# Kernel tuning notes

Hardware: AMD Instinct MI355X
Metric: run time of the kernel (lower is better)

Reference implementation:

```python
import jax, jax.numpy as jnp
import numpy as np

T = 2048        # flattened tokens (one prefill sequence)
HID = 2048      # hidden_size
NH = 32         # query heads
NKV = 4         # kv heads
HD = 128        # head_dim
THETA = 1000000.0
EPS = 1e-6


def setup_inputs() -> dict:
    key = jax.random.key(0)
    k0, k1, k2 = jax.random.split(key, 3)
    return {
        "positions": jnp.arange(T, dtype=jnp.int32),
        "hidden_states": jax.random.normal(k0, (T, HID), dtype=jnp.float32),
        "w_qkv": jax.random.normal(k1, ((NH + 2 * NKV) * HD, HID), dtype=jnp.float32) * 0.02,
        "w_o": jax.random.normal(k2, (HID, NH * HD), dtype=jnp.float32) * 0.02,
        "q_norm_w": jnp.ones((HD,), dtype=jnp.float32),
        "k_norm_w": jnp.ones((HD,), dtype=jnp.float32),
    }


def _rmsnorm(x, w):
    # per-head RMSNorm over last dim (head_dim), fp32 math
    var = jnp.mean(x * x, axis=-1, keepdims=True)
    return x * jax.lax.rsqrt(var + EPS) * w


def _rope(x, positions):
    # NeoX-style rotary embedding over full head_dim
    d = x.shape[-1]
    inv_freq = 1.0 / (THETA ** (jnp.arange(0, d, 2, dtype=jnp.float32) / d))  # [d/2]
    ang = positions.astype(jnp.float32)[:, None] * inv_freq                   # [T, d/2]
    cos = jnp.cos(ang)[:, None, :]  # [T,1,d/2]
    sin = jnp.sin(ang)[:, None, :]
    x1, x2 = jnp.split(x, 2, axis=-1)
    return jnp.concatenate([x1 * cos - x2 * sin, x2 * cos + x1 * sin], axis=-1)


def reference(positions, hidden_states, w_qkv, w_o, q_norm_w, k_norm_w):
    # fused QKV projection (no bias)
    qkv = hidden_states @ w_qkv.T                       # [T, (NH+2*NKV)*HD]
    q, k, v = jnp.split(qkv, [NH * HD, (NH + NKV) * HD], axis=-1)
    q = _rmsnorm(q.reshape(T, NH, HD), q_norm_w)        # [T,NH,HD]
    k = _rmsnorm(k.reshape(T, NKV, HD), k_norm_w)       # [T,NKV,HD]
    v = v.reshape(T, NKV, HD)
    q = _rope(q, positions)
    k = _rope(k, positions)
    # GQA: expand kv heads to query heads
    g = NH // NKV
    k = jnp.repeat(k, g, axis=1)                        # [T,NH,HD]
    v = jnp.repeat(v, g, axis=1)
    scale = HD ** -0.5
    scores = jnp.einsum('qhd,khd->hqk', q, k) * scale   # [NH,T,T]
    causal = jnp.tril(jnp.ones((T, T), dtype=bool))
    scores = jnp.where(causal[None, :, :], scores, jnp.finfo(scores.dtype).min)
    attn = jax.nn.softmax(scores, axis=-1)
    o = jnp.einsum('hqk,khd->qhd', attn, v).reshape(T, NH * HD)
    return o @ w_o.T                                    # [T,HID]
```

## Files before the change

kernel.cpp:

```cpp
#include <hip/hip_runtime.h>
#include <math.h>

#define T 2048
#define HID 2048
#define NH 32
#define NKV 4
#define HD 128
#define QKV_DIM 5120
#define OD 4096
#define C2LOG 0.12751743f
#define MFIX 6.0f

typedef _Float16 half8 __attribute__((ext_vector_type(8)));
typedef _Float16 half4v __attribute__((ext_vector_type(4)));
typedef float floatx4 __attribute__((ext_vector_type(4)));

#define GLD16(gp, lp) __builtin_amdgcn_global_load_lds( \
    (const __attribute__((address_space(1))) void*)(gp), \
    (__attribute__((address_space(3))) void*)(lp), 16, 0, 0)

__global__ __launch_bounds__(256)
void cvt_all(const float* __restrict__ h, const float* __restrict__ wq,
             const float* __restrict__ wo, _Float16* __restrict__ out) {
    size_t i = ((size_t)blockIdx.x * 256 + threadIdx.x) * 4;
    const float* src;
    size_t off;
    if (i < (size_t)T * HID)                        { src = h;  off = i; }
    else if (i < (size_t)T * HID + (size_t)QKV_DIM * HID)
                                                    { src = wq; off = i - (size_t)T * HID; }
    else                                            { src = wo; off = i - (size_t)T * HID - (size_t)QKV_DIM * HID; }
    float4 v = *(const float4*)(src + off);
    half4v o = { (_Float16)v.x, (_Float16)v.y, (_Float16)v.z, (_Float16)v.w };
    *(half4v*)(out + i) = o;
}

__global__ __launch_bounds__(256)
void gemm_sk_h(const _Float16* __restrict__ A, const _Float16* __restrict__ B,
               _Float16* __restrict__ p0, _Float16* __restrict__ p1,
               int M, int N, int K, int KS) {
    __shared__ __align__(16) _Float16 Asm[8192];
    __shared__ __align__(16) _Float16 Bsm[8192];
    int tid = threadIdx.x;
    int wave = tid >> 6, lane = tid & 63;
    int quad = lane >> 4, l16 = lane & 15;
    int m0 = blockIdx.y * 128, n0 = blockIdx.x * 128;
    int koff = blockIdx.z * KS;
    _Float16* C = blockIdx.z ? p1 : p0;
    int wm = (wave >> 1) * 64, wn = (wave & 1) * 64;
    const _Float16* Ag = A + (size_t)(m0 + (tid >> 2)) * K + koff + (tid & 3) * 8;
    const _Float16* Bg = B + (size_t)(n0 + (tid >> 2)) * K + koff + (tid & 3) * 8;
    size_t row64 = (size_t)64 * K;
    int wofs = wave * 512;
    floatx4 acc[4][4] = {};
    int nt = KS >> 5;
    GLD16(Ag, Asm + wofs);
    GLD16(Ag + row64, Asm + 2048 + wofs);
    GLD16(Bg, Bsm + wofs);
    GLD16(Bg + row64, Bsm + 2048 + wofs);
    for (int t = 0; t < nt; t++) {
        int cur = t & 1;
        if (t + 1 < nt) {
            const _Float16* Agp = Ag + (size_t)(t + 1) * 32;
            const _Float16* Bgp = Bg + (size_t)(t + 1) * 32;
            int nb = (cur ^ 1) * 4096 + wofs;
            GLD16(Agp, Asm + nb);
            GLD16(Agp + row64, Asm + nb + 2048);
            GLD16(Bgp, Bsm + nb);
            GLD16(Bgp + row64, Bsm + nb + 2048);
            asm volatile("s_waitcnt vmcnt(4)" ::: "memory");
        } else {
            asm volatile("s_waitcnt vmcnt(0)" ::: "memory");
        }
        __builtin_amdgcn_s_barrier();
        __builtin_amdgcn_sched_barrier(0);
        int pb = cur * 4096;
        half8 af[4], bf[4];
        #pragma unroll
        for (int i = 0; i < 4; i++)
            af[i] = *(const half8*)&Asm[pb + (wm + i * 16 + l16) * 32 + quad * 8];
        #pragma unroll
        for (int j = 0; j < 4; j++)
            bf[j] = *(const half8*)&Bsm[pb + (wn + j * 16 + l16) * 32 + quad * 8];
        #pragma unroll
        for (int i = 0; i < 4; i++)
            #pragma unroll
            for (int j = 0; j < 4; j++)
                acc[i][j] = __builtin_amdgcn_mfma_f32_16x16x32_f16(af[i], bf[j], acc[i][j], 0, 0, 0);
        __builtin_amdgcn_s_barrier();
    }
    #pragma unroll
    for (int i = 0; i < 4; i++) {
        int row = m0 + wm + i * 16 + quad * 4;
        #pragma unroll
        for (int j = 0; j < 4; j++) {
            int col = n0 + wn + j * 16 + l16;
            #pragma unroll
            for (int r = 0; r < 4; r++)
                C[(size_t)(row + r) * N + col] = (_Float16)acc[i][j][r];
        }
    }
}

__global__ __launch_bounds__(256)
void gemm_sk_f(const _Float16* __restrict__ A, const _Float16* __restrict__ B,
               _Float16* __restrict__ p0, _Float16* __restrict__ p1,
               _Float16* __restrict__ p2, _Float16* __restrict__ p3,
               int M, int N, int K, int KS) {
    __shared__ __align__(16) _Float16 Asm[8192];
    __shared__ __align__(16) _Float16 Bsm[8192];
    int tid = threadIdx.x;
    int wave = tid >> 6, lane = tid & 63;
    int quad = lane >> 4, l16 = lane & 15;
    int m0 = blockIdx.y * 128, n0 = blockIdx.x * 128;
    int bz = blockIdx.z;
    int koff = bz * KS;
    _Float16* C = (bz == 0) ? p0 : (bz == 1) ? p1 : (bz == 2) ? p2 : p3;
    int wm = (wave >> 1) * 64, wn = (wave & 1) * 64;
    const _Float16* Ag = A + (size_t)(m0 + (tid >> 2)) * K + koff + (tid & 3) * 8;
    const _Float16* Bg = B + (size_t)(n0 + (tid >> 2)) * K + koff + (tid & 3) * 8;
    size_t row64 = (size_t)64 * K;
    int wofs = wave * 512;
    floatx4 acc[4][4] = {};
    int nt = KS >> 5;
    GLD16(Ag, Asm + wofs);
    GLD16(Ag + row64, Asm + 2048 + wofs);
    GLD16(Bg, Bsm + wofs);
    GLD16(Bg + row64, Bsm + 2048 + wofs);
    for (int t = 0; t < nt; t++) {
        int cur = t & 1;
        if (t + 1 < nt) {
            const _Float16* Agp = Ag + (size_t)(t + 1) * 32;
            const _Float16* Bgp = Bg + (size_t)(t + 1) * 32;
            int nb = (cur ^ 1) * 4096 + wofs;
            GLD16(Agp, Asm + nb);
            GLD16(Agp + row64, Asm + nb + 2048);
            GLD16(Bgp, Bsm + nb);
            GLD16(Bgp + row64, Bsm + nb + 2048);
            asm volatile("s_waitcnt vmcnt(4)" ::: "memory");
        } else {
            asm volatile("s_waitcnt vmcnt(0)" ::: "memory");
        }
        __builtin_amdgcn_s_barrier();
        __builtin_amdgcn_sched_barrier(0);
        int pb = cur * 4096;
        half8 af[4], bf[4];
        #pragma unroll
        for (int i = 0; i < 4; i++)
            af[i] = *(const half8*)&Asm[pb + (wm + i * 16 + l16) * 32 + quad * 8];
        #pragma unroll
        for (int j = 0; j < 4; j++)
            bf[j] = *(const half8*)&Bsm[pb + (wn + j * 16 + l16) * 32 + quad * 8];
        #pragma unroll
        for (int i = 0; i < 4; i++)
            #pragma unroll
            for (int j = 0; j < 4; j++)
                acc[i][j] = __builtin_amdgcn_mfma_f32_16x16x32_f16(af[i], bf[j], acc[i][j], 0, 0, 0);
        __builtin_amdgcn_s_barrier();
    }
    #pragma unroll
    for (int i = 0; i < 4; i++) {
        int row = m0 + wm + i * 16 + quad * 4;
        #pragma unroll
        for (int j = 0; j < 4; j++) {
            int col = n0 + wn + j * 16 + l16;
            #pragma unroll
            for (int r = 0; r < 4; r++)
                C[(size_t)(row + r) * N + col] = (_Float16)acc[i][j][r];
        }
    }
}

__global__ __launch_bounds__(256)
void reduce4(const _Float16* __restrict__ p0, const _Float16* __restrict__ p1,
             const _Float16* __restrict__ p2, const _Float16* __restrict__ p3,
             float* __restrict__ out) {
    size_t i = ((size_t)blockIdx.x * 256 + threadIdx.x) * 4;
    half4v a = *(const half4v*)(p0 + i);
    half4v b = *(const half4v*)(p1 + i);
    half4v c = *(const half4v*)(p2 + i);
    half4v d = *(const half4v*)(p3 + i);
    float4 o = { (float)a.x + (float)b.x + (float)c.x + (float)d.x,
                 (float)a.y + (float)b.y + (float)c.y + (float)d.y,
                 (float)a.z + (float)b.z + (float)c.z + (float)d.z,
                 (float)a.w + (float)b.w + (float)c.w + (float)d.w };
    *(float4*)(out + i) = o;
}

__global__ __launch_bounds__(256)
void qkv_post(const _Float16* __restrict__ qp0, const _Float16* __restrict__ qp1,
              const int* __restrict__ positions,
              const float* __restrict__ qw, const float* __restrict__ kw,
              _Float16* __restrict__ Qb, _Float16* __restrict__ Kb,
              _Float16* __restrict__ Vt) {
    int t = blockIdx.x;
    int wave = threadIdx.x >> 6, lane = threadIdx.x & 63;
    float pos = (float)positions[t];
    float f = exp2f(-(float)lane * (19.9315685693241741f / 64.0f));
    float ang = pos * f;
    float s = sinf(ang), c = cosf(ang);
    const _Float16* r0 = qp0 + (size_t)t * QKV_DIM;
    const _Float16* r1 = qp1 + (size_t)t * QKV_DIM;
    for (int hh = wave; hh < NH + 2 * NKV; hh += 4) {
        float x1 = (float)r0[hh * HD + lane] + (float)r1[hh * HD + lane];
        float x2 = (float)r0[hh * HD + lane + 64] + (float)r1[hh * HD + lane + 64];
        if (hh < NH + NKV) {
            float ss = x1 * x1 + x2 * x2;
            for (int o = 1; o < 64; o <<= 1) ss += __shfl_xor(ss, o);
            float inv = rsqrtf(ss * (1.0f / HD) + 1e-6f);
            const float* w = (hh < NH) ? qw : kw;
            x1 = x1 * inv * w[lane];
            x2 = x2 * inv * w[lane + 64];
            float y1 = x1 * c - x2 * s;
            float y2 = x2 * c + x1 * s;
            _Float16* dst;
            if (hh < NH) dst = Qb + ((size_t)hh * T + t) * HD;
            else         dst = Kb + ((size_t)(hh - NH) * T + t) * HD;
            dst[lane]      = (_Float16)y1;
            dst[lane + 64] = (_Float16)y2;
        } else {
            int hk = hh - NH - NKV;
            Vt[((size_t)hk * HD + lane) * T + t]      = (_Float16)x1;
            Vt[((size_t)hk * HD + lane + 64) * T + t] = (_Float16)x2;
        }
    }
}

__global__ __launch_bounds__(256, 4)
void attn(const _Float16* __restrict__ Qb, const _Float16* __restrict__ Kb,
          const _Float16* __restrict__ Vt, _Float16* __restrict__ Ob) {
    __shared__ __align__(16) _Float16 Ksm[8192];
    __shared__ __align__(16) _Float16 Vsm[8192];
    __shared__ __align__(16) _Float16 Psm[4][1024];
    int b = blockIdx.x;
    int h = b & 31;
    int quarter = b >> 8;
    int i = (b & 255) >> 5;
    int qt = (quarter == 0) ? 31 - i : (quarter == 1) ? i
           : (quarter == 2) ? 23 - i : 8 + i;
    int hk = h >> 3;
    int tid = threadIdx.x, wave = tid >> 6, lane = tid & 63;
    int quad = lane >> 4, l16 = lane & 15;
    int q0 = qt * 64;
    int wbase = q0 + wave * 16;

    half8 aq[4];
    {
        const _Float16* qp = Qb + ((size_t)h * T + wbase + l16) * HD + quad * 8;
        #pragma unroll
        for (int dk = 0; dk < 4; dk++)
            aq[dk] = *(const half8*)(qp + dk * 32);
    }
    floatx4 o_acc[8] = {};
    float lpart[4] = {};

    int krow = tid >> 4;
    const _Float16* Kg = Kb + ((size_t)hk * T + krow) * HD + ((tid & 15) ^ (krow & 7)) * 8;
    int vrow = tid >> 3;
    const _Float16* Vg = Vt + ((size_t)hk * HD + vrow) * T + ((tid & 7) ^ (vrow & 7)) * 8;
    _Float16* KsmW = Ksm + wave * 512;
    _Float16* VsmW = Vsm + wave * 512;
    _Float16* PsmW = Psm[wave];

    int ntiles = qt + 1;
    for (int it = 0; it < ntiles; it++) {
        int kv0 = it * 64;
        __syncthreads();
        {
            const _Float16* kg = Kg + (size_t)kv0 * HD;
            const _Float16* vg = Vg + kv0;
            #pragma unroll
            for (int c = 0; c < 4; c++) {
                GLD16(kg + (size_t)c * (16 * HD), KsmW + c * 2048);
                GLD16(vg + (size_t)c * (32 * T), VsmW + c * 2048);
            }
        }
        __syncthreads();

        floatx4 sfr[4];
        #pragma unroll
        for (int sn = 0; sn < 4; sn++) {
            int row = sn * 16 + l16;
            int rs = row & 7;
            floatx4 a = {};
            #pragma unroll
            for (int dk = 0; dk < 4; dk++) {
                half8 kf = *(const half8*)&Ksm[row * 128 + ((dk * 4 + quad) ^ rs) * 8];
                a = __builtin_amdgcn_mfma_f32_16x16x32_f16(aq[dk], kf, a, 0, 0, 0);
            }
            sfr[sn] = a;
        }

        bool needmask = (it == ntiles - 1);
        int rq = wbase + quad * 4;
        #pragma unroll
        for (int sn = 0; sn < 4; sn++) {
            int kv = kv0 + sn * 16 + l16;
            #pragma unroll
            for (int r = 0; r < 4; r++) {
                float p = __builtin_amdgcn_exp2f(
                    __builtin_fmaf(sfr[sn][r], C2LOG, -MFIX));
                if (needmask) p = (kv <= rq + r) ? p : 0.0f;
                lpart[r] += p;
                int prow = quad * 4 + r;
                int cb = sn * 2 + (l16 >> 3);
                PsmW[prow * 64 + ((cb ^ (prow & 7)) * 8 + (l16 & 7))] = (_Float16)p;
            }
        }
        half8 ap0 = *(const half8*)&PsmW[l16 * 64 + ((quad ^ (l16 & 7)) * 8)];
        half8 ap1 = *(const half8*)&PsmW[l16 * 64 + (((4 + quad) ^ (l16 & 7)) * 8)];

        #pragma unroll
        for (int dn = 0; dn < 8; dn++) {
            int row = dn * 16 + l16;
            int rs = row & 7;
            half8 v0 = *(const half8*)&Vsm[row * 64 + ((quad ^ rs) * 8)];
            half8 v1 = *(const half8*)&Vsm[row * 64 + (((4 + quad) ^ rs) * 8)];
            o_acc[dn] = __builtin_amdgcn_mfma_f32_16x16x32_f16(ap0, v0, o_acc[dn], 0, 0, 0);
            o_acc[dn] = __builtin_amdgcn_mfma_f32_16x16x32_f16(ap1, v1, o_acc[dn], 0, 0, 0);
        }
    }

    #pragma unroll
    for (int o = 1; o < 16; o <<= 1)
        #pragma unroll
        for (int r = 0; r < 4; r++)
            lpart[r] += __shfl_xor(lpart[r], o);
    float linv[4];
    #pragma unroll
    for (int r = 0; r < 4; r++) linv[r] = 1.0f / lpart[r];
    int rowb = wbase + quad * 4;
    #pragma unroll
    for (int dn = 0; dn < 8; dn++) {
        int col = h * HD + dn * 16 + l16;
        #pragma unroll
        for (int r = 0; r < 4; r++)
            Ob[(size_t)(rowb + r) * OD + col] = (_Float16)(o_acc[dn][r] * linv[r]);
    }
}

extern "C" void kernel_launch(void* const* d_in, const int* in_sizes, int n_in,
                              void* d_out, int out_size, void* d_ws, size_t ws_size,
                              hipStream_t stream) {
    const int*   positions = (const int*)d_in[0];
    const float* hidden    = (const float*)d_in[1];
    const float* w_qkv     = (const float*)d_in[2];
    const float* w_o       = (const float*)d_in[3];
    const float* q_norm_w  = (const float*)d_in[4];
    const float* k_norm_w  = (const float*)d_in[5];
    float* out = (float*)d_out;

    const size_t MiB = 1048576;
    char* ws = (char*)d_ws;
    _Float16* hb    = (_Float16*)(ws);
    _Float16* wqkvb = (_Float16*)(ws + 8 * MiB);
    _Float16* wob   = (_Float16*)(ws + 28 * MiB);
    _Float16* qkvp0 = (_Float16*)(ws + 44 * MiB);
    _Float16* qkvp1 = (_Float16*)(ws + 64 * MiB);
    _Float16* Qb    = (_Float16*)(ws + 84 * MiB);
    _Float16* Kb    = (_Float16*)(ws + 100 * MiB);
    _Float16* Vt    = (_Float16*)(ws + 102 * MiB);
    _Float16* Ob    = (_Float16*)(ws + 104 * MiB);
    _Float16* op0   = (_Float16*)(ws);
    _Float16* op1   = (_Float16*)(ws + 9 * MiB);
    _Float16* op2   = (_Float16*)(ws + 44 * MiB);
    _Float16* op3   = (_Float16*)(ws + 53 * MiB);

    cvt_all<<<22528, 256, 0, stream>>>(hidden, w_qkv, w_o, hb);

    gemm_sk_h<<<dim3(QKV_DIM / 128, T / 128, 2), 256, 0, stream>>>(
        hb, wqkvb, qkvp0, qkvp1, T, QKV_DIM, HID, HID / 2);

    qkv_post<<<T, 256, 0, stream>>>(qkvp0, qkvp1, positions, q_norm_w, k_norm_w, Qb, Kb, Vt);

    attn<<<1024, 256, 0, stream>>>(Qb, Kb, Vt, Ob);

    gemm_sk_f<<<dim3(HID / 128, T / 128, 4), 256, 0, stream>>>(
        Ob, wob, op0, op1, op2, op3, T, HID, OD, OD / 4);
    reduce4<<<T * HID / 1024, 256, 0, stream>>>(op0, op1, op2, op3, out);
}
```

Baseline: 330.3 us.

## Double-buffer K/V tiles in attention and vectorize qkv_post RoPE/norm

The attention kernel now keeps two LDS buffers for K and V. It prefetches the next KV tile with global_load_lds while computing on the current one, using manual vmcnt waits and raw s_barrier in place of two __syncthreads per tile. Launch bounds drop from 4 to 2 blocks per CU to fit the doubled LDS. Separately, qkv_post processes adjacent element pairs with half2 loads and stores and builds the rotate-half partner through a lane shuffle. This overlap costs occupancy, and the hand-counted vmcnt waits could be fragile.

```diff
diff --git a/kernel.cpp b/kernel.cpp
--- a/kernel.cpp
+++ b/kernel.cpp
@@ -13,6 +13,7 @@
 
 typedef _Float16 half8 __attribute__((ext_vector_type(8)));
 typedef _Float16 half4v __attribute__((ext_vector_type(4)));
+typedef _Float16 half2v __attribute__((ext_vector_type(2)));
 typedef float floatx4 __attribute__((ext_vector_type(4)));
 
 #define GLD16(gp, lp) __builtin_amdgcn_global_load_lds( \
@@ -194,42 +195,52 @@
               _Float16* __restrict__ Vt) {
     int t = blockIdx.x;
     int wave = threadIdx.x >> 6, lane = threadIdx.x & 63;
+    int d0 = 2 * lane;
+    int j0 = d0 & 63;
     float pos = (float)positions[t];
-    float f = exp2f(-(float)lane * (19.9315685693241741f / 64.0f));
-    float ang = pos * f;
-    float s = sinf(ang), c = cosf(ang);
+    float a0 = pos * exp2f(-(float)j0 * (19.9315685693241741f / 64.0f));
+    float a1 = pos * exp2f(-(float)(j0 + 1) * (19.9315685693241741f / 64.0f));
+    float s0 = sinf(a0), c0 = cosf(a0);
+    float s1 = sinf(a1), c1 = cosf(a1);
+    float sgn = (lane < 32) ? -1.0f : 1.0f;
     const _Float16* r0 = qp0 + (size_t)t * QKV_DIM;
     const _Float16* r1 = qp1 + (size_t)t * QKV_DIM;
     for (int hh = wave; hh < NH + 2 * NKV; hh += 4) {
-        float x1 = (float)r0[hh * HD + lane] + (float)r1[hh * HD + lane];
-        float x2 = (float)r0[hh * HD + lane + 64] + (float)r1[hh * HD + lane + 64];
+        half2v u = *(const half2v*)(r0 + hh * HD + d0);
+        half2v v = *(const half2v*)(r1 + hh * HD + d0);
+        float x0 = (float)u.x + (float)v.x;
+        float x1 = (float)u.y + (float)v.y;
         if (hh < NH + NKV) {
-            float ss = x1 * x1 + x2 * x2;
+            float ss = x0 * x0 + x1 * x1;
+            #pragma unroll
             for (int o = 1; o < 64; o <<= 1) ss += __shfl_xor(ss, o);
             float inv = rsqrtf(ss * (1.0f / HD) + 1e-6f);
             const float* w = (hh < NH) ? qw : kw;
-            x1 = x1 * inv * w[lane];
-            x2 = x2 * inv * w[lane + 64];
-            float y1 = x1 * c - x2 * s;
-            float y2 = x2 * c + x1 * s;
+            float2 wv = *(const float2*)(w + d0);
+            x0 = x0 * inv * wv.x;
+            x1 = x1 * inv * wv.y;
+            float p0 = __shfl_xor(x0, 32);
+            float p1 = __shfl_xor(x1, 32);
+            float y0 = __builtin_fmaf(sgn * p0, s0, x0 * c0);
+            float y1 = __builtin_fmaf(sgn * p1, s1, x1 * c1);
             _Float16* dst;
             if (hh < NH) dst = Qb + ((size_t)hh * T + t) * HD;
             else         dst = Kb + ((size_t)(hh - NH) * T + t) * HD;
-            dst[lane]      = (_Float16)y1;
-            dst[lane + 64] = (_Float16)y2;
+            half2v y = { (_Float16)y0, (_Float16)y1 };
+            *(half2v*)(dst + d0) = y;
         } else {
             int hk = hh - NH - NKV;
-            Vt[((size_t)hk * HD + lane) * T + t]      = (_Float16)x1;
-            Vt[((size_t)hk * HD + lane + 64) * T + t] = (_Float16)x2;
-        }
-    }
-}
-
-__global__ __launch_bounds__(256, 4)
+            Vt[((size_t)hk * HD + d0) * T + t]     = (_Float16)x0;
+            Vt[((size_t)hk * HD + d0 + 1) * T + t] = (_Float16)x1;
+        }
+    }
+}
+
+__global__ __launch_bounds__(256, 2)
 void attn(const _Float16* __restrict__ Qb, const _Float16* __restrict__ Kb,
           const _Float16* __restrict__ Vt, _Float16* __restrict__ Ob) {
-    __shared__ __align__(16) _Float16 Ksm[8192];
-    __shared__ __align__(16) _Float16 Vsm[8192];
+    __shared__ __align__(16) _Float16 Ksm[2][8192];
+    __shared__ __align__(16) _Float16 Vsm[2][8192];
     __shared__ __align__(16) _Float16 Psm[4][1024];
     int b = blockIdx.x;
     int h = b & 31;
@@ -257,24 +268,38 @@
     const _Float16* Kg = Kb + ((size_t)hk * T + krow) * HD + ((tid & 15) ^ (krow & 7)) * 8;
     int vrow = tid >> 3;
     const _Float16* Vg = Vt + ((size_t)hk * HD + vrow) * T + ((tid & 7) ^ (vrow & 7)) * 8;
-    _Float16* KsmW = Ksm + wave * 512;
-    _Float16* VsmW = Vsm + wave * 512;
-    _Float16* PsmW = Psm[wave];
+    int wofs = wave * 512;
 
     int ntiles = qt + 1;
+
+    #pragma unroll
+    for (int c = 0; c < 4; c++) {
+        GLD16(Kg + (size_t)c * (16 * HD), &Ksm[0][wofs + c * 2048]);
+        GLD16(Vg + (size_t)c * (32 * T),  &Vsm[0][wofs + c * 2048]);
+    }
+
     for (int it = 0; it < ntiles; it++) {
         int kv0 = it * 64;
-        __syncthreads();
-        {
-            const _Float16* kg = Kg + (size_t)kv0 * HD;
-            const _Float16* vg = Vg + kv0;
+        int cur = it & 1;
+        if (it + 1 < ntiles) {
+            int kv1 = kv0 + 64;
+            const _Float16* kg = Kg + (size_t)kv1 * HD;
+            const _Float16* vg = Vg + kv1;
             #pragma unroll
             for (int c = 0; c < 4; c++) {
-                GLD16(kg + (size_t)c * (16 * HD), KsmW + c * 2048);
-                GLD16(vg + (size_t)c * (32 * T), VsmW + c * 2048);
+                GLD16(kg + (size_t)c * (16 * HD), &Ksm[cur ^ 1][wofs + c * 2048]);
+                GLD16(vg + (size_t)c * (32 * T),  &Vsm[cur ^ 1][wofs + c * 2048]);
             }
-        }
-        __syncthreads();
+            asm volatile("s_waitcnt vmcnt(8)" ::: "memory");
+        } else {
+            asm volatile("s_waitcnt vmcnt(0)" ::: "memory");
+        }
+        __builtin_amdgcn_s_barrier();
+        __builtin_amdgcn_sched_barrier(0);
+
+        const _Float16* Kc = Ksm[cur];
+        const _Float16* Vc = Vsm[cur];
+        _Float16* PsmW = Psm[wave];
 
         floatx4 sfr[4];
         #pragma unroll
@@ -284,7 +309,7 @@
             floatx4 a = {};
             #pragma unroll
             for (int dk = 0; dk < 4; dk++) {
-                half8 kf = *(const half8*)&Ksm[row * 128 + ((dk * 4 + quad) ^ rs) * 8];
+                half8 kf = *(const half8*)&Kc[row * 128 + ((dk * 4 + quad) ^ rs) * 8];
                 a = __builtin_amdgcn_mfma_f32_16x16x32_f16(aq[dk], kf, a, 0, 0, 0);
             }
             sfr[sn] = a;
@@ -313,11 +338,12 @@
         for (int dn = 0; dn < 8; dn++) {
             int row = dn * 16 + l16;
             int rs = row & 7;
-            half8 v0 = *(const half8*)&Vsm[row * 64 + ((quad ^ rs) * 8)];
-            half8 v1 = *(const half8*)&Vsm[row * 64 + (((4 + quad) ^ rs) * 8)];
+            half8 v0 = *(const half8*)&Vc[row * 64 + ((quad ^ rs) * 8)];
+            half8 v1 = *(const half8*)&Vc[row * 64 + (((4 + quad) ^ rs) * 8)];
             o_acc[dn] = __builtin_amdgcn_mfma_f32_16x16x32_f16(ap0, v0, o_acc[dn], 0, 0, 0);
             o_acc[dn] = __builtin_amdgcn_mfma_f32_16x16x32_f16(ap1, v1, o_acc[dn], 0, 0, 0);
         }
+        __builtin_amdgcn_s_barrier();
     }
 
     #pragma unroll
```

Measured after the change: 347.5 us. 1.05x slower.

## Double attention query tile per block to reuse K/V tiles across 32 rows per wave

Applied to the files above, without the earlier changes.

Each attention block now covers 128 query rows instead of 64, with each wave holding two 16-row query groups that share every K and V LDS tile load. The grid is halved to 512 blocks, scheduled in heavy/light order for causal load balance, and the last two KV tiles are masked. This halves K/V global loads and LDS fills per query row and amortizes barriers over more MFMA work. In exchange, register pressure roughly doubles (launch bounds drop to 2 blocks per CU), the P scratch grows, and fewer blocks may hurt occupancy and tail balance.

```diff
diff --git a/kernel.cpp b/kernel.cpp
--- a/kernel.cpp
+++ b/kernel.cpp
@@ -225,33 +225,33 @@
     }
 }
 
-__global__ __launch_bounds__(256, 4)
+__global__ __launch_bounds__(256, 2)
 void attn(const _Float16* __restrict__ Qb, const _Float16* __restrict__ Kb,
           const _Float16* __restrict__ Vt, _Float16* __restrict__ Ob) {
     __shared__ __align__(16) _Float16 Ksm[8192];
     __shared__ __align__(16) _Float16 Vsm[8192];
-    __shared__ __align__(16) _Float16 Psm[4][1024];
+    __shared__ __align__(16) _Float16 Psm[4][2048];
     int b = blockIdx.x;
-    int h = b & 31;
-    int quarter = b >> 8;
-    int i = (b & 255) >> 5;
-    int qt = (quarter == 0) ? 31 - i : (quarter == 1) ? i
-           : (quarter == 2) ? 23 - i : 8 + i;
+    int halfg = b >> 8;
+    int idx = b & 255;
+    int h = idx & 31;
+    int qi = idx >> 5;
+    int j = halfg ? qi : 15 - qi;
     int hk = h >> 3;
     int tid = threadIdx.x, wave = tid >> 6, lane = tid & 63;
     int quad = lane >> 4, l16 = lane & 15;
-    int q0 = qt * 64;
-    int wbase = q0 + wave * 16;
-
-    half8 aq[4];
-    {
-        const _Float16* qp = Qb + ((size_t)h * T + wbase + l16) * HD + quad * 8;
+    int wbase = j * 128 + wave * 32;
+
+    half8 aq[2][4];
+    #pragma unroll
+    for (int g = 0; g < 2; g++) {
+        const _Float16* qp = Qb + ((size_t)h * T + wbase + g * 16 + l16) * HD + quad * 8;
         #pragma unroll
         for (int dk = 0; dk < 4; dk++)
-            aq[dk] = *(const half8*)(qp + dk * 32);
-    }
-    floatx4 o_acc[8] = {};
-    float lpart[4] = {};
+            aq[g][dk] = *(const half8*)(qp + dk * 32);
+    }
+    floatx4 o_acc[2][8] = {};
+    float lpart[2][4] = {};
 
     int krow = tid >> 4;
     const _Float16* Kg = Kb + ((size_t)hk * T + krow) * HD + ((tid & 15) ^ (krow & 7)) * 8;
@@ -261,7 +261,7 @@
     _Float16* VsmW = Vsm + wave * 512;
     _Float16* PsmW = Psm[wave];
 
-    int ntiles = qt + 1;
+    int ntiles = 2 * j + 2;
     for (int it = 0; it < ntiles; it++) {
         int kv0 = it * 64;
         __syncthreads();
@@ -276,38 +276,42 @@
         }
         __syncthreads();
 
-        floatx4 sfr[4];
+        bool needmask = (it >= ntiles - 2);
         #pragma unroll
         for (int sn = 0; sn < 4; sn++) {
             int row = sn * 16 + l16;
             int rs = row & 7;
-            floatx4 a = {};
+            floatx4 s0 = {}, s1 = {};
             #pragma unroll
             for (int dk = 0; dk < 4; dk++) {
                 half8 kf = *(const half8*)&Ksm[row * 128 + ((dk * 4 + quad) ^ rs) * 8];
-                a = __builtin_amdgcn_mfma_f32_16x16x32_f16(aq[dk], kf, a, 0, 0, 0);
+                s0 = __builtin_amdgcn_mfma_f32_16x16x32_f16(aq[0][dk], kf, s0, 0, 0, 0);
+                s1 = __builtin_amdgcn_mfma_f32_16x16x32_f16(aq[1][dk], kf, s1, 0, 0, 0);
             }
-            sfr[sn] = a;
-        }
-
-        bool needmask = (it == ntiles - 1);
-        int rq = wbase + quad * 4;
-        #pragma unroll
-        for (int sn = 0; sn < 4; sn++) {
             int kv = kv0 + sn * 16 + l16;
-            #pragma unroll
-            for (int r = 0; r < 4; r++) {
-                float p = __builtin_amdgcn_exp2f(
-                    __builtin_fmaf(sfr[sn][r], C2LOG, -MFIX));
-                if (needmask) p = (kv <= rq + r) ? p : 0.0f;
-                lpart[r] += p;
-                int prow = quad * 4 + r;
-                int cb = sn * 2 + (l16 >> 3);
-                PsmW[prow * 64 + ((cb ^ (prow & 7)) * 8 + (l16 & 7))] = (_Float16)p;
+            int cb = sn * 2 + (l16 >> 3);
+            #pragma unroll
+            for (int g = 0; g < 2; g++) {
+                floatx4 sv = g ? s1 : s0;
+                int rqg = wbase + g * 16 + quad * 4;
+                #pragma unroll
+                for (int r = 0; r < 4; r++) {
+                    float p = __builtin_amdgcn_exp2f(
+                        __builtin_fmaf(sv[r], C2LOG, -MFIX));
+                    if (needmask) p = (kv <= rqg + r) ? p : 0.0f;
+                    lpart[g][r] += p;
+                    int prow = g * 16 + quad * 4 + r;
+                    PsmW[prow * 64 + ((cb ^ (prow & 7)) * 8 + (l16 & 7))] = (_Float16)p;
+                }
             }
         }
-        half8 ap0 = *(const half8*)&PsmW[l16 * 64 + ((quad ^ (l16 & 7)) * 8)];
-        half8 ap1 = *(const half8*)&PsmW[l16 * 64 + (((4 + quad) ^ (l16 & 7)) * 8)];
+        half8 ap[2][2];
+        #pragma unroll
+        for (int g = 0; g < 2; g++) {
+            int pr = g * 16 + l16;
+            ap[g][0] = *(const half8*)&PsmW[pr * 64 + ((quad ^ (pr & 7)) * 8)];
+            ap[g][1] = *(const half8*)&PsmW[pr * 64 + (((4 + quad) ^ (pr & 7)) * 8)];
+        }
 
         #pragma unroll
         for (int dn = 0; dn < 8; dn++) {
@@ -315,26 +319,31 @@
             int rs = row & 7;
             half8 v0 = *(const half8*)&Vsm[row * 64 + ((quad ^ rs) * 8)];
             half8 v1 = *(const half8*)&Vsm[row * 64 + (((4 + quad) ^ rs) * 8)];
-            o_acc[dn] = __builtin_amdgcn_mfma_f32_16x16x32_f16(ap0, v0, o_acc[dn], 0, 0, 0);
-            o_acc[dn] = __builtin_amdgcn_mfma_f32_16x16x32_f16(ap1, v1, o_acc[dn], 0, 0, 0);
+            o_acc[0][dn] = __builtin_amdgcn_mfma_f32_16x16x32_f16(ap[0][0], v0, o_acc[0][dn], 0, 0, 0);
+            o_acc[0][dn] = __builtin_amdgcn_mfma_f32_16x16x32_f16(ap[0][1], v1, o_acc[0][dn], 0, 0, 0);
+            o_acc[1][dn] = __builtin_amdgcn_mfma_f32_16x16x32_f16(ap[1][0], v0, o_acc[1][dn], 0, 0, 0);
+            o_acc[1][dn] = __builtin_amdgcn_mfma_f32_16x16x32_f16(ap[1][1], v1, o_acc[1][dn], 0, 0, 0);
         }
     }
 
     #pragma unroll
-    for (int o = 1; o < 16; o <<= 1)
-        #pragma unroll
-        for (int r = 0; r < 4; r++)
-            lpart[r] += __shfl_xor(lpart[r], o);
-    float linv[4];
-    #pragma unroll
-    for (int r = 0; r < 4; r++) linv[r] = 1.0f / lpart[r];
-    int rowb = wbase + quad * 4;
-    #pragma unroll
-    for (int dn = 0; dn < 8; dn++) {
-        int col = h * HD + dn * 16 + l16;
-        #pragma unroll
-        for (int r = 0; r < 4; r++)
-            Ob[(size_t)(rowb + r) * OD + col] = (_Float16)(o_acc[dn][r] * linv[r]);
+    for (int g = 0; g < 2; g++) {
+        #pragma unroll
+        for (int o = 1; o < 16; o <<= 1)
+            #pragma unroll
+            for (int r = 0; r < 4; r++)
+                lpart[g][r] += __shfl_xor(lpart[g][r], o);
+        float linv[4];
+        #pragma unroll
+        for (int r = 0; r < 4; r++) linv[r] = 1.0f / lpart[g][r];
+        int rowb = wbase + g * 16 + quad * 4;
+        #pragma unroll
+        for (int dn = 0; dn < 8; dn++) {
+            int col = h * HD + dn * 16 + l16;
+            #pragma unroll
+            for (int r = 0; r < 4; r++)
+                Ob[(size_t)(rowb + r) * OD + col] = (_Float16)(o_acc[g][dn][r] * linv[r]);
+        }
     }
 }
 
@@ -372,7 +381,7 @@
 
     qkv_post<<<T, 256, 0, stream>>>(qkvp0, qkvp1, positions, q_norm_w, k_norm_w, Qb, Kb, Vt);
 
-    attn<<<1024, 256, 0, stream>>>(Qb, Kb, Vt, Ob);
+    attn<<<512, 256, 0, stream>>>(Qb, Kb, Vt, Ob);
 
     gemm_sk_f<<<dim3(HID / 128, T / 128, 4), 256, 0, stream>>>(
         Ob, wob, op0, op1, op2, op3, T, HID, OD, OD / 4);
```

New measurement: 335.1 us. About the same (+1.5%).
